# Performance work log

Measured on AMD Instinct MI355X. Metric: run time of the kernel, lower is better.

## Reference

```python
import jax, jax.numpy as jnp
import numpy as np
from jax import lax

K = 3          # kernel_size
G = 2          # num_groups
DN = ('NHWC', 'HWIO', 'NHWC')


def _conv_same(x, w, b, groups=1):
    y = lax.conv_general_dilated(x, w, (1, 1), 'SAME',
                                 dimension_numbers=DN,
                                 feature_group_count=groups)
    return y + b


def _kernel_grid():
    off = (K - 1) / 2.0
    lin = jnp.linspace(-off, off, K, dtype=jnp.float32)
    dx, dy = jnp.meshgrid(lin, lin)              # 'xy' indexing, like tf default
    return jnp.stack([dx, dy], axis=-1).reshape(K * K, 2)  # [K2, 2] (dx, dy)


def _bilinear_sample(inp, loc):
    # inp: [B,H,W,C], loc: [B,H,W,K2,2] with (x,y) already clipped to valid range
    B, H, W, C = inp.shape
    x, y = loc[..., 0], loc[..., 1]
    x0 = jnp.floor(x); y0 = jnp.floor(y)
    x1 = jnp.clip(x0 + 1.0, 0.0, W - 1.0); x0 = jnp.clip(x0, 0.0, W - 1.0)
    y1 = jnp.clip(y0 + 1.0, 0.0, H - 1.0); y0 = jnp.clip(y0, 0.0, H - 1.0)
    # corner weights (computed from clipped coords, matching the TF code)
    wa = (x1 - x) * (y1 - y)
    wb = (x1 - x) * (y - y0)
    wc = (x - x0) * (y1 - y)
    wd = (x - x0) * (y - y0)
    x0i = x0.astype(jnp.int32); x1i = x1.astype(jnp.int32)
    y0i = y0.astype(jnp.int32); y1i = y1.astype(jnp.int32)
    flat = inp.reshape(B, H * W, C)

    def gather(yi, xi):
        idx = (yi * W + xi).reshape(B, -1, 1)               # [B, H*W*K2, 1]
        v = jnp.take_along_axis(flat, idx, axis=1)          # [B, H*W*K2, C]
        return v.reshape(B, H, W, K * K, C)

    out = (wa[..., None] * gather(y0i, x0i) + wb[..., None] * gather(y1i, x0i)
           + wc[..., None] * gather(y0i, x1i) + wd[..., None] * gather(y1i, x1i))
    return out  # [B,H,W,K2,C]


def _forward(x, off_w, off_b, dw_w, dw_b, pw_w, pw_b):
    B, H, W, C = x.shape
    Cg = C // G
    kg = _kernel_grid()                                     # [K2,2]
    gx, gy = jnp.meshgrid(jnp.arange(W, dtype=jnp.float32),
                          jnp.arange(H, dtype=jnp.float32))
    grid = jnp.stack([gx, gy], axis=-1)                     # [H,W,2] (x,y)
    outs = []
    for g in range(G):
        xi = x[..., g * Cg:(g + 1) * Cg]                    # [B,H,W,Cg]
        offsets = _conv_same(xi, off_w[g], off_b[g])        # [B,H,W,2*K2]
        offsets = offsets.reshape(B, H, W, K * K, 2)
        loc = grid[None, :, :, None, :] + kg[None, None, None] + offsets
        loc = jnp.stack([jnp.clip(loc[..., 0], 0.0, W - 1.0),
                         jnp.clip(loc[..., 1], 0.0, H - 1.0)], axis=-1)
        sampled = _bilinear_sample(xi, loc)                 # [B,H,W,K2,Cg]
        Kin = K * K * Cg
        s = sampled.reshape(B, H, W, Kin)
        s = _conv_same(s, dw_w[g], dw_b[g], groups=Kin)     # depthwise 3x3
        s = _conv_same(s, pw_w[g], pw_b[g])                 # 1x1 pointwise
        outs.append(s)
    return jnp.concatenate(outs, axis=-1)


def setup_inputs() -> dict:
    key = jax.random.key(0)
    ks = jax.random.split(key, 6)
    B, H, W, C = 4, 128, 128, 128
    Cg = C // G
    F = 128
    Fg = F // G
    Kin = K * K * Cg
    x = jax.random.normal(ks[0], (B, H, W, C), jnp.float32)
    # offset conv (zero-init in source; small random weights so offsets ~1px)
    off_w = jax.random.normal(ks[1], (G, K, K, Cg, 2 * K * K), jnp.float32) * 0.05
    off_b = jnp.zeros((G, 2 * K * K), jnp.float32)
    dw_w = jax.random.normal(ks[2], (G, K, K, 1, Kin), jnp.float32) * 0.1
    dw_b = jnp.zeros((G, Kin), jnp.float32)
    pw_w = jax.random.normal(ks[3], (G, 1, 1, Kin, Fg), jnp.float32) / np.sqrt(Kin)
    pw_b = jnp.zeros((G, Fg), jnp.float32)
    return {"x": x, "off_w": off_w, "off_b": off_b,
            "dw_w": dw_w, "dw_b": dw_b, "pw_w": pw_w, "pw_b": pw_b}


def reference(x, off_w, off_b, dw_w, dw_b, pw_w, pw_b):
    return _forward(x, off_w, off_b, dw_w, dw_b, pw_w, pw_b)
```

## Files before the change

kernel.cpp:

```cpp
#include <hip/hip_runtime.h>
#include <hip/hip_bf16.h>

#define HW 128
#define GNUM 2
#define BATCH 4
#define OBT_STRIDE (GNUM * 18 * 2 * 512)
#define PWT_FLOATS 36864
#define OBT_FLOATS 36864
#define DWP_WORDS 5184

typedef short s16x8 __attribute__((ext_vector_type(8)));
typedef _Float16 f16x8 __attribute__((ext_vector_type(8)));
typedef _Float16 f16x2 __attribute__((ext_vector_type(2)));
typedef __fp16 h16x2 __attribute__((ext_vector_type(2)));
typedef float f32x4 __attribute__((ext_vector_type(4)));
typedef float f32x2 __attribute__((ext_vector_type(2)));

__device__ inline unsigned short f2bf(float f) {
    union { float f; unsigned u; } v;
    v.f = f;
    unsigned r = (v.u + 0x7fffu + ((v.u >> 16) & 1u)) >> 16;
    return (unsigned short)r;
}
__device__ inline unsigned pk2bf(float lo, float hi) {
    __hip_bfloat162 r = __float22bfloat162_rn(float2{lo, hi});
    return *(unsigned*)&r;
}
__device__ inline float blo(unsigned u) {
    union { unsigned u; float f; } v; v.u = u << 16; return v.f;
}
__device__ inline float bhi(unsigned u) {
    union { unsigned u; float f; } v; v.u = u & 0xffff0000u; return v.f;
}
__device__ inline unsigned short f2h(float f) {
    _Float16 h = (_Float16)f;
    return *(unsigned short*)&h;
}
__device__ inline unsigned pk2h(float lo, float hi) {
    union { h16x2 h; unsigned u; } v;
    v.h = __builtin_amdgcn_cvt_pkrtz(lo, hi);
    return v.u;
}
__device__ inline f16x2 u2h(unsigned u) {
    union { unsigned u; f16x2 h; } v; v.u = u; return v.h;
}
__device__ inline unsigned h2u(f16x2 h) {
    union { unsigned u; f16x2 h; } v; v.h = h; return v.u;
}
__device__ inline int swz(int row, int off) {
    return (off & 7) | ((((off >> 3) ^ (row + (row >> 3))) & 7) << 3);
}

__global__ __launch_bounds__(256) void prep_kernel(
    const float* __restrict__ pw_w, const float* __restrict__ dw_b,
    const float* __restrict__ off_w, const float* __restrict__ dw_w,
    unsigned short* __restrict__ pwt, unsigned short* __restrict__ obt,
    unsigned* __restrict__ dwp, float* __restrict__ bias2) {
    const int g = blockIdx.y;
    const int t = threadIdx.x;
    if (blockIdx.x < 9) {
        const int j = blockIdx.x;
        const int wv = t >> 6, lane = t & 63;
        const int f = wv * 16 + (lane & 15);
        const int kbase = (lane >> 4) << 3;
#pragma unroll
        for (int ks = 0; ks < 2; ++ks)
#pragma unroll
            for (int i = 0; i < 8; ++i) {
                int kin = j * 64 + ks * 32 + kbase + i;
                pwt[((((g * 9 + j) * 4 + wv) * 2 + ks) << 9) + lane * 8 + i] =
                    f2h(pw_w[(g * 576 + kin) * 64 + f]);
            }
        for (int e = t; e < 288; e += 256) {
            int tap2 = e >> 5, cp = e & 31;
            const float* dwr = &dw_w[(g * 9 + tap2) * 576 + (j << 6) + cp * 2];
            dwp[(((g * 9 + tap2) * 9 + j) << 5) + cp] = pk2h(dwr[0], dwr[1]);
        }
    } else if (blockIdx.x < 27) {
        const int s = blockIdx.x - 9;
        const int tap = s >> 1;
        for (int e = t; e < 1024; e += 256) {
            int nt = e >> 9, le = e & 511;
            int lane = le >> 3, i = le & 7;
            int k = ((lane >> 4) << 3) + i;
            int c = ((s & 1) << 5) + k;
            int n = (nt << 4) + (lane & 15);
            float v = (n < 18) ? off_w[((g * 9 + tap) * 64 + c) * 18 + n] : 0.f;
            unsigned short hi = f2bf(v);
            unsigned short lo = f2bf(v - blo(hi));
            int idx = (((g * 18 + s) * 2 + nt) << 9) + le;
            obt[idx] = hi;
            obt[OBT_STRIDE + idx] = lo;
        }
    } else {
        __shared__ float red[256];
        const int f = t & 63, qd = t >> 6;
        float s = 0.f;
        for (int kin = qd * 144; kin < (qd + 1) * 144; ++kin)
            s += pw_w[(g * 576 + kin) * 64 + f] * dw_b[g * 576 + kin];
        red[qd * 64 + f] = s;
        __syncthreads();
        if (t < 64)
            bias2[g * 64 + t] =
                red[t] + red[64 + t] + red[128 + t] + red[192 + t];
    }
}

__global__ __launch_bounds__(256, 4) void deform_fused(
    const float* __restrict__ x, const unsigned short* __restrict__ obt,
    const float* __restrict__ off_b, const unsigned* __restrict__ dwp,
    const unsigned short* __restrict__ pwt, const float* __restrict__ bias2,
    const float* __restrict__ pw_b, float* __restrict__ out) {
    __shared__ char smem[38992];
    unsigned short* xh = (unsigned short*)smem;
    float* offs = (float*)smem;
    unsigned short* samp = (unsigned short*)smem;
    unsigned short* dwa = (unsigned short*)(smem + 12800);
    float4* wlwAll = (float4*)(smem + 20992);
    unsigned* wliAll = (unsigned*)(smem + 35392);

    const int b = blockIdx.x >> 1, g = blockIdx.x & 1;
    const int tileIdx = blockIdx.y;
    const int h0 = (tileIdx >> 4) << 3, w0 = (tileIdx & 15) << 3;
    const int t = threadIdx.x;
    const int lane = t & 63;
    const int wv = __builtin_amdgcn_readfirstlane(t >> 6);
    const int kq = (lane >> 4) << 3;
    const int col = lane & 15;
    const int rq = (lane >> 4) << 2;

    f32x4 oacc[2][2];
#pragma unroll
    for (int sl = 0; sl < 2; ++sl)
#pragma unroll
        for (int nt = 0; nt < 2; ++nt) oacc[sl][nt] = (f32x4){0.f, 0.f, 0.f, 0.f};
    int mbase[2];
#pragma unroll
    for (int sl = 0; sl < 2; ++sl) {
        int mt = wv + (sl << 2);
        int m = mt * 16 + col;
        if (mt < 7 && m < 100) {
            int opy = m / 10, opx = m - opy * 10;
            mbase[sl] = opy * 12 + opx;
        } else
            mbase[sl] = 0;
    }
    for (int q = 0; q < 2; ++q) {
        if (q) __syncthreads();
        for (int idx = t; idx < 144 * 8; idx += 256) {
            int sp = idx >> 3, cq = idx & 7;
            int sy = sp / 12, sx = sp - sy * 12;
            int gy = h0 - 2 + sy, gx = w0 - 2 + sx;
            uint2 hp = {0, 0}, lp = {0, 0};
            if ((unsigned)gy < HW && (unsigned)gx < HW) {
                const float4 v = *(const float4*)&x[(((b * HW + gy) * HW + gx)
                                                    << 7) +
                                                   (g << 6) + (q << 5) + (cq << 2)];
                hp.x = pk2bf(v.x, v.y);
                hp.y = pk2bf(v.z, v.w);
                lp.x = pk2bf(v.x - blo(hp.x), v.y - bhi(hp.x));
                lp.y = pk2bf(v.z - blo(hp.y), v.w - bhi(hp.y));
            }
            *(uint2*)&xh[sp * 64 + swz(sp, cq << 2)] = hp;
            *(uint2*)&xh[sp * 64 + swz(sp, 32 + (cq << 2))] = lp;
        }
        __syncthreads();
        for (int tap = 0; tap < 9; ++tap) {
            const int s = (tap << 1) + q;
            const int ky = tap / 3, kx = tap - ky * 3;
            const int shift = ky * 12 + kx;
            const int bidx = ((g * 18 + s) << 1) << 9;
            s16x8 bh0 = *(const s16x8*)&obt[bidx + lane * 8];
            s16x8 bh1 = *(const s16x8*)&obt[bidx + 512 + lane * 8];
            s16x8 bl0 = *(const s16x8*)&obt[OBT_STRIDE + bidx + lane * 8];
            s16x8 bl1 = *(const s16x8*)&obt[OBT_STRIDE + bidx + 512 + lane * 8];
#pragma unroll
            for (int sl = 0; sl < 2; ++sl) {
                if (wv + (sl << 2) < 7) {
                    const int m2 = mbase[sl] + shift;
                    s16x8 ah = *(const s16x8*)&xh[m2 * 64 + swz(m2, kq)];
                    s16x8 al = *(const s16x8*)&xh[m2 * 64 + swz(m2, kq + 32)];
                    oacc[sl][0] = __builtin_amdgcn_mfma_f32_16x16x32_bf16(
                        ah, bh0, oacc[sl][0], 0, 0, 0);
                    oacc[sl][1] = __builtin_amdgcn_mfma_f32_16x16x32_bf16(
                        ah, bh1, oacc[sl][1], 0, 0, 0);
                    oacc[sl][0] = __builtin_amdgcn_mfma_f32_16x16x32_bf16(
                        al, bh0, oacc[sl][0], 0, 0, 0);
                    oacc[sl][1] = __builtin_amdgcn_mfma_f32_16x16x32_bf16(
                        al, bh1, oacc[sl][1], 0, 0, 0);
                    oacc[sl][0] = __builtin_amdgcn_mfma_f32_16x16x32_bf16(
                        ah, bl0, oacc[sl][0], 0, 0, 0);
                    oacc[sl][1] = __builtin_amdgcn_mfma_f32_16x16x32_bf16(
                        ah, bl1, oacc[sl][1], 0, 0, 0);
                }
            }
        }
    }
    __syncthreads();
#pragma unroll
    for (int sl = 0; sl < 2; ++sl) {
        int mt = wv + (sl << 2);
        if (mt < 7) {
#pragma unroll
            for (int nt = 0; nt < 2; ++nt) {
                int o = (nt << 4) + col;
                if (o < 18) {
                    float ob = off_b[g * 18 + o];
#pragma unroll
                    for (int i = 0; i < 4; ++i) {
                        int m = mt * 16 + rq + i;
                        if (m < 100) offs[m * 18 + o] = oacc[sl][nt][i] + ob;
                    }
                }
            }
        }
    }
    __syncthreads();
    for (int e = t; e < 900; e += 256) {
        const int jj = e / 100, sp = e - jj * 100;
        const int jy = jj / 3, jx = jj - jy * 3;
        const int spy = sp / 10, spx = sp - spy * 10;
        const int gy = h0 - 1 + spy, gx = w0 - 1 + spx;
        float4 w4 = {0.f, 0.f, 0.f, 0.f};
        unsigned wp = (unsigned)(b << 21);
        if ((unsigned)gy < HW && (unsigned)gx < HW) {
            const float ox = offs[sp * 18 + 2 * jj];
            const float oy = offs[sp * 18 + 2 * jj + 1];
            float xf = fminf(fmaxf((float)(gx + jx - 1) + ox, 0.f), 127.f);
            float yf = fminf(fmaxf((float)(gy + jy - 1) + oy, 0.f), 127.f);
            float x0 = floorf(xf), y0 = floorf(yf);
            float x1 = fminf(x0 + 1.f, 127.f);
            float y1 = fminf(y0 + 1.f, 127.f);
            w4.x = (x1 - xf) * (y1 - yf);
            w4.y = (x1 - xf) * (yf - y0);
            w4.z = (xf - x0) * (y1 - yf);
            w4.w = (xf - x0) * (yf - y0);
            const int x0i = (int)x0, y0i = (int)y0;
            wp = (unsigned)(((b * HW + y0i) * HW + x0i) << 7) |
                 (unsigned)((int)x1 - x0i) |
                 ((unsigned)((int)y1 - y0i) << 1);
        }
        wlwAll[jj * 100 + sp] = w4;
        wliAll[jj * 100 + sp] = wp;
    }
    __syncthreads();

    const int fb = wv << 4;
    const int p = lane;
    const int ayp = p >> 3, axp = p & 7;
    const int grp = t >> 4, sl16 = t & 15;
    const int prow = ayp * 10 + axp;

    int aoff[9][2];
#pragma unroll
    for (int t2 = 0; t2 < 9; ++t2) {
        const int ky = t2 / 3, kx = t2 - ky * 3;
        const int row = prow + ky * 10 + kx;
#pragma unroll
        for (int cq = 0; cq < 2; ++cq)
            aoff[t2][cq] = row * 64 + swz(row, fb + (cq << 3));
    }
    int doff[2];
#pragma unroll
    for (int cq = 0; cq < 2; ++cq) doff[cq] = p * 64 + swz(p, fb + (cq << 3));
    int boff[2][4];
#pragma unroll
    for (int ks = 0; ks < 2; ++ks)
#pragma unroll
        for (int mt = 0; mt < 4; ++mt) {
            const int row = mt * 16 + col;
            boff[ks][mt] = row * 64 + swz(row, ks * 32 + kq);
        }
    int soff[7];
#pragma unroll
    for (int it = 0; it < 7; ++it) {
        const int sp_ = (it << 4) + grp;
        soff[it] = sp_ * 64 + swz(sp_, sl16 << 2);
    }

    const float bs = bias2[g * 64 + fb + col] + pw_b[g * 64 + fb + col];
    f32x4 acc[4];
#pragma unroll
    for (int mt = 0; mt < 4; ++mt) acc[mt] = (f32x4){bs, bs, bs, bs};

    for (int j = 0; j < 9; ++j) {
        f16x8 bfr[2];
#pragma unroll
        for (int ks = 0; ks < 2; ++ks)
            bfr[ks] = *(const f16x8*)&pwt[((((g * 9 + j) * 4 + wv) * 2 + ks)
                                           << 9) + lane * 8];
        for (int it = 0; it < 7; ++it) {
            const int sp = (it << 4) + grp;
            if (sp < 100) {
                const float4 w4 = wlwAll[j * 100 + sp];
                const unsigned wp = wliAll[j * 100 + sp];
                const float* xa = x + (wp & 0xFFFFFF80u) + (g << 6) +
                                  (sl16 << 2);
                const int xo = (int)((wp & 1u) << 7);
                const int yo = (int)((wp & 2u) << 13);
                const float4 va = *(const float4*)xa;
                const float4 vb = *(const float4*)(xa + yo);
                const float4 vc = *(const float4*)(xa + xo);
                const float4 vd = *(const float4*)(xa + xo + yo);
                f32x2 a01 = {va.x, va.y}, b01 = {vb.x, vb.y};
                f32x2 c01 = {vc.x, vc.y}, d01 = {vd.x, vd.y};
                f32x2 a23 = {va.z, va.w}, b23 = {vb.z, vb.w};
                f32x2 c23 = {vc.z, vc.w}, d23 = {vd.z, vd.w};
                f32x2 r01 = w4.x * a01 + w4.y * b01 + w4.z * c01 + w4.w * d01;
                f32x2 r23 = w4.x * a23 + w4.y * b23 + w4.z * c23 + w4.w * d23;
                uint2 pk;
                pk.x = pk2h(r01.x, r01.y);
                pk.y = pk2h(r23.x, r23.y);
                *(uint2*)&samp[soff[it]] = pk;
            }
        }
        __syncthreads();
#pragma unroll
        for (int cq = 0; cq < 2; ++cq) {
            const int c8 = fb + (cq << 3);
            f16x2 d0 = {0, 0}, d1 = {0, 0}, d2 = {0, 0}, d3 = {0, 0};
#pragma unroll
            for (int t2 = 0; t2 < 9; ++t2) {
                const uint4 hv = *(const uint4*)&samp[aoff[t2][cq]];
                const uint4 wq =
                    *(const uint4*)&dwp[(((g * 9 + t2) * 9 + j) << 5) +
                                        (c8 >> 1)];
                d0 = u2h(hv.x) * u2h(wq.x) + d0;
                d1 = u2h(hv.y) * u2h(wq.y) + d1;
                d2 = u2h(hv.z) * u2h(wq.z) + d2;
                d3 = u2h(hv.w) * u2h(wq.w) + d3;
            }
            uint4 pk;
            pk.x = h2u(d0);
            pk.y = h2u(d1);
            pk.z = h2u(d2);
            pk.w = h2u(d3);
            *(uint4*)&dwa[doff[cq]] = pk;
        }
        __syncthreads();
#pragma unroll
        for (int ks = 0; ks < 2; ++ks)
#pragma unroll
            for (int mt = 0; mt < 4; ++mt) {
                f16x8 af = *(const f16x8*)&dwa[boff[ks][mt]];
                acc[mt] = __builtin_amdgcn_mfma_f32_16x16x32_f16(
                    af, bfr[ks], acc[mt], 0, 0, 0);
            }
    }
#pragma unroll
    for (int mt = 0; mt < 4; ++mt)
#pragma unroll
        for (int i = 0; i < 4; ++i) {
            int m = mt * 16 + rq + i;
            out[((b * HW + h0 + (m >> 3)) * HW + (w0 + (m & 7))) * 128 +
                (g << 6) + fb + col] = acc[mt][i];
        }
}

extern "C" void kernel_launch(void* const* d_in, const int* in_sizes, int n_in,
                              void* d_out, int out_size, void* d_ws,
                              size_t ws_size, hipStream_t stream) {
    const float* x = (const float*)d_in[0];
    const float* off_w = (const float*)d_in[1];
    const float* off_b = (const float*)d_in[2];
    const float* dw_w = (const float*)d_in[3];
    const float* dw_b = (const float*)d_in[4];
    const float* pw_w = (const float*)d_in[5];
    const float* pw_b = (const float*)d_in[6];

    float* wsf = (float*)d_ws;
    unsigned short* pwt = (unsigned short*)wsf;
    unsigned short* obt = (unsigned short*)(wsf + PWT_FLOATS);
    unsigned* dwp = (unsigned*)(wsf + PWT_FLOATS + OBT_FLOATS);
    float* bias2 = wsf + PWT_FLOATS + OBT_FLOATS + DWP_WORDS;

    prep_kernel<<<dim3(28, GNUM), dim3(256), 0, stream>>>(pw_w, dw_b, off_w,
                                                          dw_w, pwt, obt, dwp,
                                                          bias2);
    deform_fused<<<dim3(BATCH * GNUM, 256), dim3(256), 0, stream>>>(
        x, obt, off_b, dwp, pwt, bias2, pw_b, (float*)d_out);
}
```

Baseline: 194.6 us.

## Halve spatial tile height to 4x8 outputs per block, doubling grid

Shrinks each block's output tile from 8x8 to 4x8 pixels and launches twice as many blocks. Shared-memory buffers, halo loads, offset-conv MFMA tiling, the sampling loop and the pointwise MFMA loop are all resized to match. The aim is lower LDS use and more blocks for occupancy and load balance across CUs. In exchange the halo recompute ratio rises (6x12 input rows for 4 output rows) and per-block overhead is amortized over less work.

```diff
diff --git a/kernel.cpp b/kernel.cpp
--- a/kernel.cpp
+++ b/kernel.cpp
@@ -111,17 +111,17 @@
     const float* __restrict__ off_b, const unsigned* __restrict__ dwp,
     const unsigned short* __restrict__ pwt, const float* __restrict__ bias2,
     const float* __restrict__ pw_b, float* __restrict__ out) {
-    __shared__ char smem[38992];
+    __shared__ char smem[33024];
     unsigned short* xh = (unsigned short*)smem;
     float* offs = (float*)smem;
     unsigned short* samp = (unsigned short*)smem;
-    unsigned short* dwa = (unsigned short*)(smem + 12800);
-    float4* wlwAll = (float4*)(smem + 20992);
-    unsigned* wliAll = (unsigned*)(smem + 35392);
+    unsigned short* dwa = (unsigned short*)(smem + 7680);
+    float4* wlwAll = (float4*)(smem + 12288);
+    unsigned* wliAll = (unsigned*)(smem + 20928);
 
     const int b = blockIdx.x >> 1, g = blockIdx.x & 1;
     const int tileIdx = blockIdx.y;
-    const int h0 = (tileIdx >> 4) << 3, w0 = (tileIdx & 15) << 3;
+    const int h0 = (tileIdx >> 4) << 2, w0 = (tileIdx & 15) << 3;
     const int t = threadIdx.x;
     const int lane = t & 63;
     const int wv = __builtin_amdgcn_readfirstlane(t >> 6);
@@ -129,25 +129,20 @@
     const int col = lane & 15;
     const int rq = (lane >> 4) << 2;
 
-    f32x4 oacc[2][2];
-#pragma unroll
-    for (int sl = 0; sl < 2; ++sl)
-#pragma unroll
-        for (int nt = 0; nt < 2; ++nt) oacc[sl][nt] = (f32x4){0.f, 0.f, 0.f, 0.f};
-    int mbase[2];
-#pragma unroll
-    for (int sl = 0; sl < 2; ++sl) {
-        int mt = wv + (sl << 2);
-        int m = mt * 16 + col;
-        if (mt < 7 && m < 100) {
+    f32x4 oacc[2];
+#pragma unroll
+    for (int nt = 0; nt < 2; ++nt) oacc[nt] = (f32x4){0.f, 0.f, 0.f, 0.f};
+    int mbase = 0;
+    {
+        int m = wv * 16 + col;
+        if (m < 60) {
             int opy = m / 10, opx = m - opy * 10;
-            mbase[sl] = opy * 12 + opx;
-        } else
-            mbase[sl] = 0;
+            mbase = opy * 12 + opx;
+        }
     }
     for (int q = 0; q < 2; ++q) {
         if (q) __syncthreads();
-        for (int idx = t; idx < 144 * 8; idx += 256) {
+        for (int idx = t; idx < 96 * 8; idx += 256) {
             int sp = idx >> 3, cq = idx & 7;
             int sy = sp / 12, sx = sp - sy * 12;
             int gy = h0 - 2 + sy, gx = w0 - 2 + sx;
@@ -174,50 +169,39 @@
             s16x8 bh1 = *(const s16x8*)&obt[bidx + 512 + lane * 8];
             s16x8 bl0 = *(const s16x8*)&obt[OBT_STRIDE + bidx + lane * 8];
             s16x8 bl1 = *(const s16x8*)&obt[OBT_STRIDE + bidx + 512 + lane * 8];
-#pragma unroll
-            for (int sl = 0; sl < 2; ++sl) {
-                if (wv + (sl << 2) < 7) {
-                    const int m2 = mbase[sl] + shift;
-                    s16x8 ah = *(const s16x8*)&xh[m2 * 64 + swz(m2, kq)];
-                    s16x8 al = *(const s16x8*)&xh[m2 * 64 + swz(m2, kq + 32)];
-                    oacc[sl][0] = __builtin_amdgcn_mfma_f32_16x16x32_bf16(
-                        ah, bh0, oacc[sl][0], 0, 0, 0);
-                    oacc[sl][1] = __builtin_amdgcn_mfma_f32_16x16x32_bf16(
-                        ah, bh1, oacc[sl][1], 0, 0, 0);
-                    oacc[sl][0] = __builtin_amdgcn_mfma_f32_16x16x32_bf16(
-                        al, bh0, oacc[sl][0], 0, 0, 0);
-                    oacc[sl][1] = __builtin_amdgcn_mfma_f32_16x16x32_bf16(
-                        al, bh1, oacc[sl][1], 0, 0, 0);
-                    oacc[sl][0] = __builtin_amdgcn_mfma_f32_16x16x32_bf16(
-                        ah, bl0, oacc[sl][0], 0, 0, 0);
-                    oacc[sl][1] = __builtin_amdgcn_mfma_f32_16x16x32_bf16(
-                        ah, bl1, oacc[sl][1], 0, 0, 0);
-                }
-            }
+            const int m2 = mbase + shift;
+            s16x8 ah = *(const s16x8*)&xh[m2 * 64 + swz(m2, kq)];
+            s16x8 al = *(const s16x8*)&xh[m2 * 64 + swz(m2, kq + 32)];
+            oacc[0] = __builtin_amdgcn_mfma_f32_16x16x32_bf16(ah, bh0,
+                                                              oacc[0], 0, 0, 0);
+            oacc[1] = __builtin_amdgcn_mfma_f32_16x16x32_bf16(ah, bh1,
+                                                              oacc[1], 0, 0, 0);
+            oacc[0] = __builtin_amdgcn_mfma_f32_16x16x32_bf16(al, bh0,
+                                                              oacc[0], 0, 0, 0);
+            oacc[1] = __builtin_amdgcn_mfma_f32_16x16x32_bf16(al, bh1,
+                                                              oacc[1], 0, 0, 0);
+            oacc[0] = __builtin_amdgcn_mfma_f32_16x16x32_bf16(ah, bl0,
+                                                              oacc[0], 0, 0, 0);
+            oacc[1] = __builtin_amdgcn_mfma_f32_16x16x32_bf16(ah, bl1,
+                                                              oacc[1], 0, 0, 0);
         }
     }
     __syncthreads();
 #pragma unroll
-    for (int sl = 0; sl < 2; ++sl) {
-        int mt = wv + (sl << 2);
-        if (mt < 7) {
-#pragma unroll
-            for (int nt = 0; nt < 2; ++nt) {
-                int o = (nt << 4) + col;
-                if (o < 18) {
-                    float ob = off_b[g * 18 + o];
-#pragma unroll
-                    for (int i = 0; i < 4; ++i) {
-                        int m = mt * 16 + rq + i;
-                        if (m < 100) offs[m * 18 + o] = oacc[sl][nt][i] + ob;
-                    }
-                }
+    for (int nt = 0; nt < 2; ++nt) {
+        int o = (nt << 4) + col;
+        if (o < 18) {
+            float ob = off_b[g * 18 + o];
+#pragma unroll
+            for (int i = 0; i < 4; ++i) {
+                int m = wv * 16 + rq + i;
+                if (m < 60) offs[m * 18 + o] = oacc[nt][i] + ob;
             }
         }
     }
     __syncthreads();
-    for (int e = t; e < 900; e += 256) {
-        const int jj = e / 100, sp = e - jj * 100;
+    for (int e = t; e < 540; e += 256) {
+        const int jj = e / 60, sp = e - jj * 60;
         const int jy = jj / 3, jx = jj - jy * 3;
         const int spy = sp / 10, spx = sp - spy * 10;
         const int gy = h0 - 1 + spy, gx = w0 - 1 + spx;
@@ -240,60 +224,59 @@
                  (unsigned)((int)x1 - x0i) |
                  ((unsigned)((int)y1 - y0i) << 1);
         }
-        wlwAll[jj * 100 + sp] = w4;
-        wliAll[jj * 100 + sp] = wp;
+        wlwAll[jj * 60 + sp] = w4;
+        wliAll[jj * 60 + sp] = wp;
     }
     __syncthreads();
 
     const int fb = wv << 4;
-    const int p = lane;
+    const int p = lane & 31;
+    const int acq = lane >> 5;
     const int ayp = p >> 3, axp = p & 7;
     const int grp = t >> 4, sl16 = t & 15;
     const int prow = ayp * 10 + axp;
-
-    int aoff[9][2];
+    const int c8 = fb + (acq << 3);
+
+    int aoff[9];
 #pragma unroll
     for (int t2 = 0; t2 < 9; ++t2) {
         const int ky = t2 / 3, kx = t2 - ky * 3;
         const int row = prow + ky * 10 + kx;
-#pragma unroll
-        for (int cq = 0; cq < 2; ++cq)
-            aoff[t2][cq] = row * 64 + swz(row, fb + (cq << 3));
-    }
-    int doff[2];
-#pragma unroll
-    for (int cq = 0; cq < 2; ++cq) doff[cq] = p * 64 + swz(p, fb + (cq << 3));
-    int boff[2][4];
+        aoff[t2] = row * 64 + swz(row, c8);
+    }
+    const int doff = p * 64 + swz(p, c8);
+    int boff[2][2];
 #pragma unroll
     for (int ks = 0; ks < 2; ++ks)
 #pragma unroll
-        for (int mt = 0; mt < 4; ++mt) {
+        for (int mt = 0; mt < 2; ++mt) {
             const int row = mt * 16 + col;
             boff[ks][mt] = row * 64 + swz(row, ks * 32 + kq);
         }
-    int soff[7];
-#pragma unroll
-    for (int it = 0; it < 7; ++it) {
+    int soff[4];
+#pragma unroll
+    for (int it = 0; it < 4; ++it) {
         const int sp_ = (it << 4) + grp;
         soff[it] = sp_ * 64 + swz(sp_, sl16 << 2);
     }
 
     const float bs = bias2[g * 64 + fb + col] + pw_b[g * 64 + fb + col];
-    f32x4 acc[4];
-#pragma unroll
-    for (int mt = 0; mt < 4; ++mt) acc[mt] = (f32x4){bs, bs, bs, bs};
-
+    f32x4 acc[2];
+#pragma unroll
+    for (int mt = 0; mt < 2; ++mt) acc[mt] = (f32x4){bs, bs, bs, bs};
+
+    const int dwpBase = (g * 9 * 9) << 5;
     for (int j = 0; j < 9; ++j) {
         f16x8 bfr[2];
 #pragma unroll
         for (int ks = 0; ks < 2; ++ks)
             bfr[ks] = *(const f16x8*)&pwt[((((g * 9 + j) * 4 + wv) * 2 + ks)
                                            << 9) + lane * 8];
-        for (int it = 0; it < 7; ++it) {
+        for (int it = 0; it < 4; ++it) {
             const int sp = (it << 4) + grp;
-            if (sp < 100) {
-                const float4 w4 = wlwAll[j * 100 + sp];
-                const unsigned wp = wliAll[j * 100 + sp];
+            if (sp < 60) {
+                const float4 w4 = wlwAll[j * 60 + sp];
+                const unsigned wp = wliAll[j * 60 + sp];
                 const float* xa = x + (wp & 0xFFFFFF80u) + (g << 6) +
                                   (sl16 << 2);
                 const int xo = (int)((wp & 1u) << 7);
@@ -315,15 +298,13 @@
             }
         }
         __syncthreads();
-#pragma unroll
-        for (int cq = 0; cq < 2; ++cq) {
-            const int c8 = fb + (cq << 3);
+        {
             f16x2 d0 = {0, 0}, d1 = {0, 0}, d2 = {0, 0}, d3 = {0, 0};
 #pragma unroll
             for (int t2 = 0; t2 < 9; ++t2) {
-                const uint4 hv = *(const uint4*)&samp[aoff[t2][cq]];
+                const uint4 hv = *(const uint4*)&samp[aoff[t2]];
                 const uint4 wq =
-                    *(const uint4*)&dwp[(((g * 9 + t2) * 9 + j) << 5) +
+                    *(const uint4*)&dwp[dwpBase + (((t2 * 9 + j) << 5)) +
                                         (c8 >> 1)];
                 d0 = u2h(hv.x) * u2h(wq.x) + d0;
                 d1 = u2h(hv.y) * u2h(wq.y) + d1;
@@ -335,20 +316,20 @@
             pk.y = h2u(d1);
             pk.z = h2u(d2);
             pk.w = h2u(d3);
-            *(uint4*)&dwa[doff[cq]] = pk;
+            *(uint4*)&dwa[doff] = pk;
         }
         __syncthreads();
 #pragma unroll
         for (int ks = 0; ks < 2; ++ks)
 #pragma unroll
-            for (int mt = 0; mt < 4; ++mt) {
+            for (int mt = 0; mt < 2; ++mt) {
                 f16x8 af = *(const f16x8*)&dwa[boff[ks][mt]];
                 acc[mt] = __builtin_amdgcn_mfma_f32_16x16x32_f16(
                     af, bfr[ks], acc[mt], 0, 0, 0);
             }
     }
 #pragma unroll
-    for (int mt = 0; mt < 4; ++mt)
+    for (int mt = 0; mt < 2; ++mt)
 #pragma unroll
         for (int i = 0; i < 4; ++i) {
             int m = mt * 16 + rq + i;
@@ -377,6 +358,6 @@
     prep_kernel<<<dim3(28, GNUM), dim3(256), 0, stream>>>(pw_w, dw_b, off_w,
                                                           dw_w, pwt, obt, dwp,
                                                           bias2);
-    deform_fused<<<dim3(BATCH * GNUM, 256), dim3(256), 0, stream>>>(
+    deform_fused<<<dim3(BATCH * GNUM, 512), dim3(256), 0, stream>>>(
         x, obt, off_b, dwp, pwt, bias2, pw_b, (float*)d_out);
 }
```

Measured after the change: 257.6 us. 1.32x slower.
